# Kernel optimization log

Hardware: AMD Instinct MI355X
Metric: run time of the kernel (lower is better)

The kernel has to match this reference:

```python
import jax, jax.numpy as jnp
import numpy as np

B, H, S, D = 2, 16, 2048, 128
BLOCK_N = 64          # key-block size used by the Triton inner loop (BLOCK_N<=HEAD_DIM configs)
CAUSAL = True
NEG = -1000000.0      # kernel masks with -1e6, not -inf
LOG2E = 1.44269504


def _round_away(x):
    # tl.math.floor(|x| + 0.5) * sign(x): round half away from zero
    return jnp.floor(jnp.abs(x) + 0.5) * jnp.where(x >= 0, 1.0, -1.0)


def _quant_per_token(x):
    # per-(B,H,S) symmetric int8 quantization (values kept in fp32; exact, since |q|<=127)
    amax = jnp.maximum(jnp.max(jnp.abs(x), axis=-1), 1e-8)
    scale = amax / 127.0
    xq = jnp.clip(_round_away(x / scale[..., None]), -127.0, 127.0)
    return xq, scale


def _quant_per_head(v):
    # per-(B,H) symmetric int8 quantization
    amax = jnp.maximum(jnp.max(jnp.abs(v), axis=(-2, -1)), 1e-8)
    scale = amax / 127.0
    vq = jnp.clip(_round_away(v / scale[..., None, None]), -127.0, 127.0)
    return vq, scale


def _forward(q, k, v, sm_scale):
    q_q, q_s = _quant_per_token(q)   # [B,H,S,D], [B,H,S]
    k_q, k_s = _quant_per_token(k)
    v_q, v_s = _quant_per_head(v)    # [B,H,S,D], [B,H]

    nb = S // BLOCK_N
    k_blk = k_q.reshape(B, H, nb, BLOCK_N, D).transpose(2, 0, 1, 3, 4)   # [nb,B,H,Bn,D]
    ks_blk = k_s.reshape(B, H, nb, BLOCK_N).transpose(2, 0, 1, 3)        # [nb,B,H,Bn]
    v_blk = v_q.reshape(B, H, nb, BLOCK_N, D).transpose(2, 0, 1, 3, 4)   # [nb,B,H,Bn,D]
    cols = jnp.arange(S, dtype=jnp.int32).reshape(nb, BLOCK_N)
    rows = jnp.arange(S, dtype=jnp.int32)

    qk_scale = sm_scale * LOG2E
    vs_term = v_s[:, :, None, None] / 127.0  # [B,H,1,1]

    def step(carry, xs):
        m, l, acc = carry
        kb, ksb, vb, cb = xs
        # int8 QK^T dequantized: exact in fp32 (|sum| <= 127*127*128 < 2^24)
        qk = jnp.einsum('bhsd,bhnd->bhsn', q_q, kb)
        qk = qk * q_s[..., None] * ksb[:, :, None, :] * qk_scale
        if CAUSAL:
            qk = jnp.where(rows[:, None] >= cb[None, :], qk, NEG)
        m_new = jnp.maximum(m, jnp.max(qk, axis=-1))
        p = jnp.exp2(qk - m_new[..., None])
        # online quantization of probabilities at block-local running max (as in kernel)
        p_q = jnp.floor(p * 127.0 + 0.5)
        alpha = jnp.exp2(m - m_new)
        l = l * alpha + jnp.sum(p, axis=-1)
        acc = acc * alpha[..., None] + jnp.einsum('bhsn,bhnd->bhsd', p_q, vb) * vs_term
        return (m_new, l, acc), None

    m0 = jnp.full((B, H, S), -jnp.inf, dtype=jnp.float32)
    l0 = jnp.ones((B, H, S), dtype=jnp.float32)   # killed by alpha=exp2(-inf)=0 at first block
    acc0 = jnp.zeros((B, H, S, D), dtype=jnp.float32)
    (m, l, acc), _ = jax.lax.scan(jax.checkpoint(step), (m0, l0, acc0),
                                  (k_blk, ks_blk, v_blk, cols))
    return acc / l[..., None]


def setup_inputs() -> dict:
    key = jax.random.key(0)
    kq, kk, kv = jax.random.split(key, 3)
    q = jax.random.normal(kq, (B, H, S, D), dtype=jnp.float32)
    k = jax.random.normal(kk, (B, H, S, D), dtype=jnp.float32)
    v = jax.random.normal(kv, (B, H, S, D), dtype=jnp.float32)
    sm_scale = jnp.float32(1.0 / np.sqrt(D))
    return {"q": q, "k": k, "v": v, "sm_scale": sm_scale}


def reference(q, k, v, sm_scale):
    return _forward(q, k, v, sm_scale)
```

## Files before the change

kernel.cpp:

```cpp
#include <hip/hip_runtime.h>

#define S_LEN 2048
#define D_DIM 128
#define NBH   32
#define LOG2E 1.44269504f
#define NEGM  -1000000.0f

typedef __bf16 bf16x8 __attribute__((ext_vector_type(8)));
typedef short  s16x8  __attribute__((ext_vector_type(8)));
typedef float  f32x4  __attribute__((ext_vector_type(4)));
typedef float  f32x16 __attribute__((ext_vector_type(16)));
typedef unsigned int u32x4 __attribute__((ext_vector_type(4)));

static __device__ __forceinline__ unsigned short f32_to_bf16_bits_exact(float f) {
    return (unsigned short)(__float_as_uint(f) >> 16);
}
static __device__ __forceinline__ float round_away(float t) {
    float r = floorf(fabsf(t) + 0.5f);
    return (t >= 0.0f) ? r : -r;
}
static __device__ __forceinline__ unsigned int pq_pack(float p0, float p1) {
    float a = floorf(fmaf(p0, 127.0f, 0.5f));
    float b = floorf(fmaf(p1, 127.0f, 0.5f));
    return __builtin_amdgcn_perm(__float_as_uint(b), __float_as_uint(a), 0x07060302);
}

__global__ __launch_bounds__(256) void quant_qkv_kernel(
    const float* __restrict__ q, const float* __restrict__ k,
    const float* __restrict__ v,
    unsigned short* __restrict__ qq, unsigned short* __restrict__ kq,
    float* __restrict__ qs, float* __restrict__ ks,
    unsigned int* __restrict__ vab)
{
    if (blockIdx.x < 16384) {
        const int R = NBH * S_LEN;
        int w   = blockIdx.x * 8 + (threadIdx.x >> 5);
        int l32 = threadIdx.x & 31;
        const float* src; unsigned short* dq; float* ds; int row;
        if (w < R) { src = q; dq = qq; ds = qs; row = w; }
        else       { src = k; dq = kq; ds = ks; row = w - R; }
        size_t base = (size_t)row * D_DIM + l32 * 4;
        float4 x = *(const float4*)(src + base);
        float amax = fmaxf(fmaxf(fabsf(x.x), fabsf(x.y)), fmaxf(fabsf(x.z), fabsf(x.w)));
        #pragma unroll
        for (int m = 1; m < 32; m <<= 1) amax = fmaxf(amax, __shfl_xor(amax, m));
        float scale = fmaxf(amax, 1e-8f) / 127.0f;
        ushort4 o;
        o.x = f32_to_bf16_bits_exact(fminf(fmaxf(round_away(x.x / scale), -127.0f), 127.0f));
        o.y = f32_to_bf16_bits_exact(fminf(fmaxf(round_away(x.y / scale), -127.0f), 127.0f));
        o.z = f32_to_bf16_bits_exact(fminf(fmaxf(round_away(x.z / scale), -127.0f), 127.0f));
        o.w = f32_to_bf16_bits_exact(fminf(fmaxf(round_away(x.w / scale), -127.0f), 127.0f));
        *(ushort4*)(dq + base) = o;
        if (l32 == 0) ds[row] = scale;
    } else {
        int bid2 = blockIdx.x - 16384;
        int bh = bid2 >> 3, blk = bid2 & 7;
        const float4* base = (const float4*)(v + (size_t)bh * S_LEN * D_DIM) + blk * 8192;
        int t = threadIdx.x;
        float am = 0.0f;
        #pragma unroll
        for (int i = 0; i < 32; ++i) {
            float4 x = base[t + i * 256];
            am = fmaxf(am, fmaxf(fmaxf(fabsf(x.x), fabsf(x.y)), fmaxf(fabsf(x.z), fabsf(x.w))));
        }
        #pragma unroll
        for (int m = 1; m < 64; m <<= 1) am = fmaxf(am, __shfl_xor(am, m));
        __shared__ float red[4];
        if ((t & 63) == 0) red[t >> 6] = am;
        __syncthreads();
        if (t == 0) {
            float a = fmaxf(fmaxf(red[0], red[1]), fmaxf(red[2], red[3]));
            atomicMax(&vab[bh], __float_as_uint(a));
        }
    }
}

__global__ __launch_bounds__(256) void vtq_kernel(const float* __restrict__ v,
                                                  const unsigned int* __restrict__ vab,
                                                  unsigned short* __restrict__ vT)
{
    __shared__ unsigned short tileT[128][72];
    int bh = blockIdx.x >> 5, sb = blockIdx.x & 31;
    float scale = fmaxf(__uint_as_float(vab[bh]), 1e-8f) / 127.0f;
    int t = threadIdx.x;
    const float* src = v + ((size_t)bh * S_LEN + sb * 64) * D_DIM;
    #pragma unroll
    for (int it = 0; it < 8; ++it) {
        int c = t + it * 256;
        int rs = c >> 5, c4 = (c & 31) * 4;
        float4 x = *(const float4*)(src + rs * D_DIM + c4);
        float vals[4] = {x.x, x.y, x.z, x.w};
        #pragma unroll
        for (int u = 0; u < 4; ++u) {
            float r = fminf(fmaxf(round_away(vals[u] / scale), -127.0f), 127.0f);
            tileT[c4 + u][rs] = f32_to_bf16_bits_exact(r);
        }
    }
    __syncthreads();
    unsigned short* dst = vT + (size_t)bh * D_DIM * S_LEN + sb * 64;
    #pragma unroll
    for (int it = 0; it < 4; ++it) {
        int c = t + it * 256;
        int d = c >> 3, c8 = (c & 7) * 8;
        *(s16x8*)(dst + (size_t)d * S_LEN + c8) = *(const s16x8*)&tileT[d][c8];
    }
}

__global__ __launch_bounds__(512, 4) void attn_kernel(
    const unsigned short* __restrict__ qq,
    const unsigned short* __restrict__ kq,
    const unsigned short* __restrict__ vT,
    const float* __restrict__ qs,
    const float* __restrict__ ks,
    const unsigned int* __restrict__ vab,
    const float* __restrict__ smp,
    float* __restrict__ out)
{
    extern __shared__ char smem[];

    const int tid  = threadIdx.x;
    const int lane = tid & 63;
    const int wid  = tid >> 6;
    const int w4   = wid & 3;
    const int half = wid >> 2;
    const int c32  = lane & 31;
    const int hi   = lane >> 5;
    const int t8   = tid & 255;

    char*   KbH  = smem + half * 8192;
    char*   VbH  = smem + 16384 + half * 8192;
    float*  ksl  = (float*)(smem + 32768);
    float2* ML   = (float2*)(smem + 34816);
    char*   Qlds = smem + 40960;
    float*  Ol   = (float*)smem;

    const int bid = blockIdx.x;
    const int g   = bid >> 5;
    const int qb  = (g < 8) ? (15 - g) : (g - 8);
    const int bh  = bid & 31;

    const float qk_scale = smp[0] * LOG2E;
    const float vscale   = fmaxf(__uint_as_float(vab[bh]), 1e-8f) / 127.0f;
    const float vs_term  = vscale / 127.0f;

    const int   q  = qb * 128 + c32 * 4 + w4;
    const float qf = qs[(size_t)bh * S_LEN + q] * qk_scale;

    const char* kqb = (const char*)(kq + (size_t)bh * S_LEN * D_DIM);
    const char* vtb = (const char*)(vT + (size_t)bh * D_DIM * S_LEN);

    ((f32x4*)ksl)[tid] = ((const f32x4*)(ks + (size_t)bh * S_LEN))[tid];
    {
        const char* qqb = (const char*)(qq + ((size_t)bh * S_LEN + qb * 128) * D_DIM);
        #pragma unroll
        for (int it = 0; it < 4; ++it) {
            int L = (tid + it * 512) * 16;
            int w = L >> 13, Lw = L & 8191;
            int r = Lw >> 8, x = Lw & 255;
            int col = x ^ ((r & 15) << 4);
            *(s16x8*)(Qlds + L) = *(const s16x8*)(qqb + (r * 4 + w) * 256 + col);
        }
    }

    int kOff[2], vOff[2], lOff[2];
    #pragma unroll
    for (int it = 0; it < 2; ++it) {
        int L = (t8 + it * 256) * 16;
        lOff[it] = L;
        int r = L >> 8, x = L & 255;
        int c = x ^ ((r & 15) << 4);
        kOff[it] = (half * 32 + r) * 256 + c;
        vOff[it] = ((c >> 6) * 32 + r) * (S_LEN * 2) + half * 64 + (c & 63);
    }

    float mrow = -100.0f;
    float lrow = 0.0f;
    f32x16 oacc0, oacc1, oacc2, oacc3;
    #pragma unroll
    for (int i = 0; i < 16; ++i) { oacc0[i] = 0.f; oacc1[i] = 0.f; oacc2[i] = 0.f; oacc3[i] = 0.f; }

    const int swz = (c32 & 15) << 4;
    const char* aBase = KbH + c32 * 256;
    const char* bBase = Qlds + w4 * 8192 + c32 * 256;
    const char* vBase = VbH + c32 * 256;

    const int jn = 2 * qb + 2;
    for (int j = 0; j < jn; ++j) {
        const int jb = j * 64;
        s16x8 kr0 = *(const s16x8*)(kqb + jb * 256 + kOff[0]);
        s16x8 kr1 = *(const s16x8*)(kqb + jb * 256 + kOff[1]);
        s16x8 vr0 = *(const s16x8*)(vtb + jb * 2   + vOff[0]);
        s16x8 vr1 = *(const s16x8*)(vtb + jb * 2   + vOff[1]);
        __syncthreads();
        *(s16x8*)(KbH + lOff[0]) = kr0;
        *(s16x8*)(KbH + lOff[1]) = kr1;
        *(s16x8*)(VbH + lOff[0]) = vr0;
        *(s16x8*)(VbH + lOff[1]) = vr1;
        __syncthreads();

        f32x16 sc;
        #pragma unroll
        for (int i = 0; i < 16; ++i) sc[i] = 0.f;
        #pragma unroll
        for (int st = 0; st < 8; ++st) {
            int cB = (st * 32 + hi * 16) ^ swz;
            bf16x8 a = __builtin_bit_cast(bf16x8, *(const s16x8*)(aBase + cB));
            bf16x8 b = __builtin_bit_cast(bf16x8, *(const s16x8*)(bBase + cB));
            sc = __builtin_amdgcn_mfma_f32_32x32x16_bf16(a, b, sc, 0, 0, 0);
        }

        const int  jbh = jb + half * 32;
        const bool need_mask = (jbh + 31 > qb * 128 + w4);
        float mhA = -3.0e38f, mhB = -3.0e38f;
        #pragma unroll
        for (int gg = 0; gg < 4; ++gg) {
            f32x4 kv = *(const f32x4*)&ksl[jbh + gg * 8 + hi * 4];
            #pragma unroll
            for (int i = 0; i < 4; ++i) {
                int r = gg * 4 + i;
                float c  = qf * kv[i];
                float tv = fmaf(sc[r], c, -mrow);
                if (need_mask) tv = (q >= jbh + gg * 8 + i + hi * 4) ? tv : NEGM;
                sc[r] = tv;
                if (i & 1) mhB = fmaxf(mhB, tv);
                else       mhA = fmaxf(mhA, tv);
            }
        }
        float mh     = fmaxf(mhA, mhB);
        float vmax_t = fmaxf(mh, __shfl_xor(mh, 32));

        if (__any(vmax_t > 1.0f)) {
            float sh    = fmaxf(vmax_t, 0.0f);
            float alpha = exp2f(-sh);
            mrow += sh;
            #pragma unroll
            for (int r = 0; r < 16; ++r) sc[r] -= sh;
            oacc0 *= alpha; oacc1 *= alpha; oacc2 *= alpha; oacc3 *= alpha;
            lrow  *= alpha;
        }

        float ts[8];
        #pragma unroll
        for (int r = 0; r < 8; ++r) {
            sc[r]     = exp2f(sc[r]);
            sc[r + 8] = exp2f(sc[r + 8]);
            ts[r] = sc[r] + sc[r + 8];
        }
        #pragma unroll
        for (int stp = 4; stp >= 1; stp >>= 1)
            #pragma unroll
            for (int r = 0; r < stp; ++r) ts[r] += ts[r + stp];
        lrow += ts[0] + __shfl_xor(ts[0], 32);

        unsigned int W[8];
        #pragma unroll
        for (int gg = 0; gg < 4; ++gg) {
            W[gg*2+0] = pq_pack(sc[gg*4+0], sc[gg*4+1]);
            W[gg*2+1] = pq_pack(sc[gg*4+2], sc[gg*4+3]);
        }
        #pragma unroll
        for (int s = 0; s < 2; ++s) {
            asm("v_permlane32_swap_b32 %0, %1" : "+v"(W[s*4+0]), "+v"(W[s*4+2]));
            asm("v_permlane32_swap_b32 %0, %1" : "+v"(W[s*4+1]), "+v"(W[s*4+3]));
        }
        #pragma unroll
        for (int s = 0; s < 2; ++s) {
            u32x4 uw; uw.x = W[s*4+0]; uw.y = W[s*4+1]; uw.z = W[s*4+2]; uw.w = W[s*4+3];
            bf16x8 bfrag = __builtin_bit_cast(bf16x8, uw);
            int cb = s * 32 + hi * 16;
            bf16x8 va;
            va = __builtin_bit_cast(bf16x8, *(const s16x8*)(vBase + ((cb +   0) ^ swz)));
            oacc0 = __builtin_amdgcn_mfma_f32_32x32x16_bf16(va, bfrag, oacc0, 0, 0, 0);
            va = __builtin_bit_cast(bf16x8, *(const s16x8*)(vBase + ((cb +  64) ^ swz)));
            oacc1 = __builtin_amdgcn_mfma_f32_32x32x16_bf16(va, bfrag, oacc1, 0, 0, 0);
            va = __builtin_bit_cast(bf16x8, *(const s16x8*)(vBase + ((cb + 128) ^ swz)));
            oacc2 = __builtin_amdgcn_mfma_f32_32x32x16_bf16(va, bfrag, oacc2, 0, 0, 0);
            va = __builtin_bit_cast(bf16x8, *(const s16x8*)(vBase + ((cb + 192) ^ swz)));
            oacc3 = __builtin_amdgcn_mfma_f32_32x32x16_bf16(va, bfrag, oacc3, 0, 0, 0);
        }
    }

    __syncthreads();
    if (hi == 0) { float2 ml2; ml2.x = mrow; ml2.y = lrow; ML[half * 128 + w4 * 32 + c32] = ml2; }
    __syncthreads();
    float2 mo  = ML[(1 - half) * 128 + w4 * 32 + c32];
    float  mfin = fmaxf(mrow, mo.x);
    float  bs  = exp2f(mrow - mfin);
    float  bo  = exp2f(mo.x - mfin);
    float  lfin = lrow * bs + mo.y * bo;
    const float inv = bs * vs_term / lfin;

    for (int pass = 0; pass < 2; ++pass) {
        __syncthreads();
        if (half == 0 && (w4 >> 1) == pass) {
            float* reg = Ol + (w4 & 1) * 4224 + c32 * 132;
            #pragma unroll
            for (int r = 0; r < 16; ++r) {
                int drow = (r & 3) + 8 * (r >> 2) + 4 * hi;
                reg[drow]      = oacc0[r] * inv;
                reg[drow + 32] = oacc1[r] * inv;
                reg[drow + 64] = oacc2[r] * inv;
                reg[drow + 96] = oacc3[r] * inv;
            }
        }
        __syncthreads();
        if (half == 1 && (w4 >> 1) == pass) {
            float* reg = Ol + (w4 & 1) * 4224 + c32 * 132;
            #pragma unroll
            for (int r = 0; r < 16; ++r) {
                int drow = (r & 3) + 8 * (r >> 2) + 4 * hi;
                reg[drow]      += oacc0[r] * inv;
                reg[drow + 32] += oacc1[r] * inv;
                reg[drow + 64] += oacc2[r] * inv;
                reg[drow + 96] += oacc3[r] * inv;
            }
        }
        __syncthreads();
        #pragma unroll
        for (int it = 0; it < 4; ++it) {
            int idx = tid + it * 512;
            int w2  = idx >> 10;
            int rem = idx & 1023;
            int row = rem >> 5, c4 = rem & 31;
            f32x4 v4 = *(const f32x4*)(Ol + w2 * 4224 + row * 132 + c4 * 4);
            int qr = qb * 128 + row * 4 + pass * 2 + w2;
            *(f32x4*)(out + ((size_t)bh * S_LEN + qr) * D_DIM + c4 * 4) = v4;
        }
    }
}

extern "C" void kernel_launch(void* const* d_in, const int* in_sizes, int n_in,
                              void* d_out, int out_size, void* d_ws, size_t ws_size,
                              hipStream_t stream)
{
    const float* q  = (const float*)d_in[0];
    const float* k  = (const float*)d_in[1];
    const float* v  = (const float*)d_in[2];
    const float* sm = (const float*)d_in[3];

    if (ws_size < (size_t)50857000) return;
    char* ws = (char*)d_ws;
    unsigned short* qq = (unsigned short*)(ws);
    unsigned short* kq = (unsigned short*)(ws + (1u << 24));
    unsigned short* vT = (unsigned short*)(ws + (2u << 24));
    float*          qs = (float*)(ws + (3u << 24));
    float*          ks = (float*)(ws + (3u << 24) + 262144);
    unsigned int*  vab = (unsigned int*)(ws + (3u << 24) + 524288);
    float*         out = (float*)d_out;

    hipFuncSetAttribute((const void*)attn_kernel,
                        hipFuncAttributeMaxDynamicSharedMemorySize, 73728);

    hipMemsetAsync(vab, 0, NBH * sizeof(unsigned int), stream);
    quant_qkv_kernel<<<dim3(16640), dim3(256), 0, stream>>>(q, k, v, qq, kq, qs, ks, vab);
    vtq_kernel<<<dim3(1024), dim3(256), 0, stream>>>(v, vab, vT);
    attn_kernel<<<dim3(512), dim3(512), 73728, stream>>>(qq, kq, vT, qs, ks, vab, sm, out);
}
```

Before: 125.8 us.

## Fuse Q quantization into attention and split long causal rows across blocks

Q quantization moves from the separate prepass into the attention kernel, which now reads fp32 Q, quantizes it into LDS and stores the per-row scales there. This removes the qq/qs round trip through global memory. Query blocks 9-15, the longest causal rows, are each split into two key-range chunks processed by separate workgroups (736 blocks instead of 512) to even out work. The chunk that finishes last, found through an atomic ticket, merges both partial outputs using the stored m/l values. In exchange this adds scratch traffic, atomics and merge work, and each workgroup repeats the Q quantization.

```diff
diff --git a/kernel.cpp b/kernel.cpp
--- a/kernel.cpp
+++ b/kernel.cpp
@@ -11,6 +11,7 @@
 typedef float  f32x4  __attribute__((ext_vector_type(4)));
 typedef float  f32x16 __attribute__((ext_vector_type(16)));
 typedef unsigned int u32x4 __attribute__((ext_vector_type(4)));
+typedef unsigned int u32x2 __attribute__((ext_vector_type(2)));
 
 static __device__ __forceinline__ unsigned short f32_to_bf16_bits_exact(float f) {
     return (unsigned short)(__float_as_uint(f) >> 16);
@@ -25,22 +26,16 @@
     return __builtin_amdgcn_perm(__float_as_uint(b), __float_as_uint(a), 0x07060302);
 }
 
-__global__ __launch_bounds__(256) void quant_qkv_kernel(
-    const float* __restrict__ q, const float* __restrict__ k,
-    const float* __restrict__ v,
-    unsigned short* __restrict__ qq, unsigned short* __restrict__ kq,
-    float* __restrict__ qs, float* __restrict__ ks,
+__global__ __launch_bounds__(256) void quant_kv_kernel(
+    const float* __restrict__ k, const float* __restrict__ v,
+    unsigned short* __restrict__ kq, float* __restrict__ ks,
     unsigned int* __restrict__ vab)
 {
-    if (blockIdx.x < 16384) {
-        const int R = NBH * S_LEN;
-        int w   = blockIdx.x * 8 + (threadIdx.x >> 5);
+    if (blockIdx.x < 8192) {
+        int row = blockIdx.x * 8 + (threadIdx.x >> 5);
         int l32 = threadIdx.x & 31;
-        const float* src; unsigned short* dq; float* ds; int row;
-        if (w < R) { src = q; dq = qq; ds = qs; row = w; }
-        else       { src = k; dq = kq; ds = ks; row = w - R; }
         size_t base = (size_t)row * D_DIM + l32 * 4;
-        float4 x = *(const float4*)(src + base);
+        float4 x = *(const float4*)(k + base);
         float amax = fmaxf(fmaxf(fabsf(x.x), fabsf(x.y)), fmaxf(fabsf(x.z), fabsf(x.w)));
         #pragma unroll
         for (int m = 1; m < 32; m <<= 1) amax = fmaxf(amax, __shfl_xor(amax, m));
@@ -50,10 +45,10 @@
         o.y = f32_to_bf16_bits_exact(fminf(fmaxf(round_away(x.y / scale), -127.0f), 127.0f));
         o.z = f32_to_bf16_bits_exact(fminf(fmaxf(round_away(x.z / scale), -127.0f), 127.0f));
         o.w = f32_to_bf16_bits_exact(fminf(fmaxf(round_away(x.w / scale), -127.0f), 127.0f));
-        *(ushort4*)(dq + base) = o;
-        if (l32 == 0) ds[row] = scale;
+        *(ushort4*)(kq + base) = o;
+        if (l32 == 0) ks[row] = scale;
     } else {
-        int bid2 = blockIdx.x - 16384;
+        int bid2 = blockIdx.x - 8192;
         int bh = bid2 >> 3, blk = bid2 & 7;
         const float4* base = (const float4*)(v + (size_t)bh * S_LEN * D_DIM) + blk * 8192;
         int t = threadIdx.x;
@@ -107,14 +102,16 @@
 }
 
 __global__ __launch_bounds__(512, 4) void attn_kernel(
-    const unsigned short* __restrict__ qq,
+    const float* __restrict__ qsrc,
     const unsigned short* __restrict__ kq,
     const unsigned short* __restrict__ vT,
-    const float* __restrict__ qs,
     const float* __restrict__ ks,
     const unsigned int* __restrict__ vab,
     const float* __restrict__ smp,
-    float* __restrict__ out)
+    float* __restrict__ out,
+    float* __restrict__ U1,
+    float2* __restrict__ mlbuf,
+    unsigned int* __restrict__ tickets)
 {
     extern __shared__ char smem[];
 
@@ -134,33 +131,63 @@
     char*   Qlds = smem + 40960;
     float*  Ol   = (float*)smem;
 
-    const int bid = blockIdx.x;
-    const int g   = bid >> 5;
-    const int qb  = (g < 8) ? (15 - g) : (g - 8);
-    const int bh  = bid & 31;
+    int rem = (int)blockIdx.x, qb = 0, chunk = -1, bh = 0;
+    {
+        bool fnd = false;
+        for (int L = 18; L >= 2 && !fnd; --L) {
+            if (L >= 10 && L <= 16) {
+                if (rem < 64) { qb = L - 1; chunk = rem >> 5; bh = rem & 31; fnd = true; }
+                else rem -= 64;
+            }
+            if (!fnd && !(L & 1)) {
+                int qu = (L >> 1) - 1;
+                if (qu <= 8) {
+                    if (rem < 32) { qb = qu; chunk = -1; bh = rem & 31; fnd = true; }
+                    else rem -= 32;
+                }
+            }
+        }
+    }
+    int j0 = 0, jEnd = 2 * qb + 2;
+    if (chunk == 0) jEnd = qb + 1;
+    else if (chunk == 1) j0 = qb + 1;
+    const int pair = (qb - 9) * 32 + bh;
 
     const float qk_scale = smp[0] * LOG2E;
     const float vscale   = fmaxf(__uint_as_float(vab[bh]), 1e-8f) / 127.0f;
     const float vs_term  = vscale / 127.0f;
 
-    const int   q  = qb * 128 + c32 * 4 + w4;
-    const float qf = qs[(size_t)bh * S_LEN + q] * qk_scale;
-
     const char* kqb = (const char*)(kq + (size_t)bh * S_LEN * D_DIM);
     const char* vtb = (const char*)(vT + (size_t)bh * D_DIM * S_LEN);
 
     ((f32x4*)ksl)[tid] = ((const f32x4*)(ks + (size_t)bh * S_LEN))[tid];
+    float* qsl = (float*)smem;
     {
-        const char* qqb = (const char*)(qq + ((size_t)bh * S_LEN + qb * 128) * D_DIM);
-        #pragma unroll
-        for (int it = 0; it < 4; ++it) {
-            int L = (tid + it * 512) * 16;
-            int w = L >> 13, Lw = L & 8191;
-            int r = Lw >> 8, x = Lw & 255;
-            int col = x ^ ((r & 15) << 4);
-            *(s16x8*)(Qlds + L) = *(const s16x8*)(qqb + (r * 4 + w) * 256 + col);
-        }
-    }
+        const float* qg = qsrc + ((size_t)bh * S_LEN + qb * 128) * D_DIM;
+        int l32 = tid & 31;
+        #pragma unroll
+        for (int p = 0; p < 8; ++p) {
+            int row = p * 16 + (tid >> 5);
+            f32x4 x = *(const f32x4*)(qg + (size_t)row * D_DIM + l32 * 4);
+            float am = fmaxf(fmaxf(fabsf(x[0]), fabsf(x[1])), fmaxf(fabsf(x[2]), fabsf(x[3])));
+            #pragma unroll
+            for (int m = 1; m < 32; m <<= 1) am = fmaxf(am, __shfl_xor(am, m));
+            float scale = fmaxf(am, 1e-8f) / 127.0f;
+            if (l32 == 0) qsl[row] = scale;
+            unsigned short b0 = f32_to_bf16_bits_exact(fminf(fmaxf(round_away(x[0] / scale), -127.0f), 127.0f));
+            unsigned short b1 = f32_to_bf16_bits_exact(fminf(fmaxf(round_away(x[1] / scale), -127.0f), 127.0f));
+            unsigned short b2 = f32_to_bf16_bits_exact(fminf(fmaxf(round_away(x[2] / scale), -127.0f), 127.0f));
+            unsigned short b3 = f32_to_bf16_bits_exact(fminf(fmaxf(round_away(x[3] / scale), -127.0f), 127.0f));
+            u32x2 pk; pk.x = (unsigned int)b0 | ((unsigned int)b1 << 16);
+            pk.y = (unsigned int)b2 | ((unsigned int)b3 << 16);
+            int base = (row & 3) * 8192 + (row >> 2) * 256;
+            int off  = (l32 * 8) ^ (((row >> 2) & 15) << 4);
+            *(u32x2*)(Qlds + base + off) = pk;
+        }
+    }
+    __syncthreads();
+    const int   q  = qb * 128 + c32 * 4 + w4;
+    const float qf = qsl[c32 * 4 + w4] * qk_scale;
 
     int kOff[2], vOff[2], lOff[2];
     #pragma unroll
@@ -184,8 +211,7 @@
     const char* bBase = Qlds + w4 * 8192 + c32 * 256;
     const char* vBase = VbH + c32 * 256;
 
-    const int jn = 2 * qb + 2;
-    for (int j = 0; j < jn; ++j) {
+    for (int j = j0; j < jEnd; ++j) {
         const int jb = j * 64;
         s16x8 kr0 = *(const s16x8*)(kqb + jb * 256 + kOff[0]);
         s16x8 kr1 = *(const s16x8*)(kqb + jb * 256 + kOff[1]);
@@ -288,7 +314,15 @@
     float  bs  = exp2f(mrow - mfin);
     float  bo  = exp2f(mo.x - mfin);
     float  lfin = lrow * bs + mo.y * bo;
-    const float inv = bs * vs_term / lfin;
+
+    if (chunk >= 0 && half == 0 && hi == 0) {
+        float2 t; t.x = mfin; t.y = lfin;
+        mlbuf[(size_t)pair * 256 + chunk * 128 + (c32 * 4 + w4)] = t;
+    }
+
+    const float inv = (chunk < 0) ? (bs * vs_term / lfin) : bs;
+    float* dstBase = (chunk == 1) ? (U1 + (size_t)pair * 16384)
+                                  : (out + ((size_t)bh * S_LEN + qb * 128) * D_DIM);
 
     for (int pass = 0; pass < 2; ++pass) {
         __syncthreads();
@@ -320,11 +354,44 @@
         for (int it = 0; it < 4; ++it) {
             int idx = tid + it * 512;
             int w2  = idx >> 10;
-            int rem = idx & 1023;
-            int row = rem >> 5, c4 = rem & 31;
+            int rem2 = idx & 1023;
+            int row = rem2 >> 5, c4 = rem2 & 31;
             f32x4 v4 = *(const f32x4*)(Ol + w2 * 4224 + row * 132 + c4 * 4);
-            int qr = qb * 128 + row * 4 + pass * 2 + w2;
-            *(f32x4*)(out + ((size_t)bh * S_LEN + qr) * D_DIM + c4 * 4) = v4;
+            int lr = row * 4 + pass * 2 + w2;
+            *(f32x4*)(dstBase + (size_t)lr * D_DIM + c4 * 4) = v4;
+        }
+    }
+
+    if (chunk >= 0) {
+        __syncthreads();
+        int* flg = (int*)(smem + 34816);
+        if (tid == 0) {
+            __threadfence();
+            unsigned int old = __hip_atomic_fetch_add(&tickets[pair], 1u,
+                                 __ATOMIC_ACQ_REL, __HIP_MEMORY_SCOPE_AGENT);
+            flg[0] = (int)old;
+        }
+        __syncthreads();
+        if (flg[0] == 1) {
+            __threadfence();
+            const float2* mp = mlbuf + (size_t)pair * 256;
+            float* orows = out + ((size_t)bh * S_LEN + qb * 128) * D_DIM;
+            const float* U1p = U1 + (size_t)pair * 16384;
+            #pragma unroll
+            for (int it = 0; it < 8; ++it) {
+                int vec = tid + it * 512;
+                int row = vec >> 5;
+                float2 a = mp[row], b = mp[128 + row];
+                float ms = fmaxf(a.x, b.x);
+                float w0 = exp2f(a.x - ms), w1 = exp2f(b.x - ms);
+                float scl = vs_term / (w0 * a.y + w1 * b.y);
+                f32x4 u0 = ((const f32x4*)orows)[vec];
+                f32x4 u1 = ((const f32x4*)U1p)[vec];
+                f32x4 r;
+                #pragma unroll
+                for (int c = 0; c < 4; ++c) r[c] = (u0[c] * w0 + u1[c] * w1) * scl;
+                ((f32x4*)orows)[vec] = r;
+            }
         }
     }
 }
@@ -340,19 +407,21 @@
 
     if (ws_size < (size_t)50857000) return;
     char* ws = (char*)d_ws;
-    unsigned short* qq = (unsigned short*)(ws);
-    unsigned short* kq = (unsigned short*)(ws + (1u << 24));
-    unsigned short* vT = (unsigned short*)(ws + (2u << 24));
-    float*          qs = (float*)(ws + (3u << 24));
-    float*          ks = (float*)(ws + (3u << 24) + 262144);
-    unsigned int*  vab = (unsigned int*)(ws + (3u << 24) + 524288);
+    unsigned short* kq = (unsigned short*)(ws);
+    unsigned short* vT = (unsigned short*)(ws + (1u << 24));
+    float*          ks = (float*)(ws + (2u << 24));
+    unsigned int*  vab = (unsigned int*)(ws + (2u << 24) + 262144);
+    unsigned int* tick = (unsigned int*)(ws + (2u << 24) + 263168);
+    float2*         ml = (float2*)(ws + (2u << 24) + 264192);
+    float*          U1 = (float*)(ws + (2u << 24) + 1048576);
     float*         out = (float*)d_out;
 
     hipFuncSetAttribute((const void*)attn_kernel,
                         hipFuncAttributeMaxDynamicSharedMemorySize, 73728);
 
-    hipMemsetAsync(vab, 0, NBH * sizeof(unsigned int), stream);
-    quant_qkv_kernel<<<dim3(16640), dim3(256), 0, stream>>>(q, k, v, qq, kq, qs, ks, vab);
+    hipMemsetAsync(ws + (2u << 24) + 262144, 0, 2048, stream);
+    quant_kv_kernel<<<dim3(8448), dim3(256), 0, stream>>>(k, v, kq, ks, vab);
     vtq_kernel<<<dim3(1024), dim3(256), 0, stream>>>(v, vab, vT);
-    attn_kernel<<<dim3(512), dim3(512), 73728, stream>>>(qq, kq, vT, qs, ks, vab, sm, out);
-}
+    attn_kernel<<<dim3(736), dim3(512), 73728, stream>>>(q, kq, vT, ks, vab, sm,
+                                                         out, U1, ml, tick);
+}
```

New measurement: 219.0 us. 74.1% more time.

## Double key block size to 128 and prefetch next K/V block into registers

Applied to the files above, without the earlier changes.

Each iteration of the attention kernel now processes a 128-key block, 64 keys per half, with two score accumulators per wave. This halves the number of barrier-synchronised iterations. Global loads for the next K/V block are issued into registers before the compute of the current block, to overlap memory latency with MFMA work. Only the last block takes the masked path, and the block ordering becomes a simple descending schedule. The cost is more LDS (about 106 KB) and more registers, with launch bounds reduced to 2 blocks per SM, which lowers occupancy.

```diff
diff --git a/kernel.cpp b/kernel.cpp
--- a/kernel.cpp
+++ b/kernel.cpp
@@ -106,7 +106,7 @@
     }
 }
 
-__global__ __launch_bounds__(512, 4) void attn_kernel(
+__global__ __launch_bounds__(512, 2) void attn_kernel(
     const unsigned short* __restrict__ qq,
     const unsigned short* __restrict__ kq,
     const unsigned short* __restrict__ vT,
@@ -127,16 +127,15 @@
     const int hi   = lane >> 5;
     const int t8   = tid & 255;
 
-    char*   KbH  = smem + half * 8192;
-    char*   VbH  = smem + 16384 + half * 8192;
-    float*  ksl  = (float*)(smem + 32768);
-    float2* ML   = (float2*)(smem + 34816);
-    char*   Qlds = smem + 40960;
+    char*   KbH  = smem + half * 16384;
+    char*   VbH  = smem + 32768 + half * 16384;
+    float*  ksl  = (float*)(smem + 65536);
+    float2* ML   = (float2*)(smem + 73728);
+    char*   Qlds = smem + 75776;
     float*  Ol   = (float*)smem;
 
     const int bid = blockIdx.x;
-    const int g   = bid >> 5;
-    const int qb  = (g < 8) ? (15 - g) : (g - 8);
+    const int qb  = 15 - (bid >> 5);
     const int bh  = bid & 31;
 
     const float qk_scale = smp[0] * LOG2E;
@@ -162,15 +161,17 @@
         }
     }
 
-    int kOff[2], vOff[2], lOff[2];
-    #pragma unroll
-    for (int it = 0; it < 2; ++it) {
+    int kOff[4], vOff[4], lOff[4];
+    #pragma unroll
+    for (int it = 0; it < 4; ++it) {
         int L = (t8 + it * 256) * 16;
         lOff[it] = L;
         int r = L >> 8, x = L & 255;
         int c = x ^ ((r & 15) << 4);
-        kOff[it] = (half * 32 + r) * 256 + c;
-        vOff[it] = ((c >> 6) * 32 + r) * (S_LEN * 2) + half * 64 + (c & 63);
+        kOff[it] = (half * 64 + r) * 256 + c;
+        int rho = L >> 9, xv = L & 511;
+        int cv  = xv ^ ((rho & 15) << 4);
+        vOff[it] = ((cv >> 7) * 32 + rho) * (S_LEN * 2) + half * 128 + (cv & 127);
     }
 
     float mrow = -100.0f;
@@ -182,48 +183,65 @@
     const int swz = (c32 & 15) << 4;
     const char* aBase = KbH + c32 * 256;
     const char* bBase = Qlds + w4 * 8192 + c32 * 256;
-    const char* vBase = VbH + c32 * 256;
-
-    const int jn = 2 * qb + 2;
-    for (int j = 0; j < jn; ++j) {
-        const int jb = j * 64;
-        s16x8 kr0 = *(const s16x8*)(kqb + jb * 256 + kOff[0]);
-        s16x8 kr1 = *(const s16x8*)(kqb + jb * 256 + kOff[1]);
-        s16x8 vr0 = *(const s16x8*)(vtb + jb * 2   + vOff[0]);
-        s16x8 vr1 = *(const s16x8*)(vtb + jb * 2   + vOff[1]);
-        __syncthreads();
-        *(s16x8*)(KbH + lOff[0]) = kr0;
-        *(s16x8*)(KbH + lOff[1]) = kr1;
-        *(s16x8*)(VbH + lOff[0]) = vr0;
-        *(s16x8*)(VbH + lOff[1]) = vr1;
-        __syncthreads();
-
-        f32x16 sc;
-        #pragma unroll
-        for (int i = 0; i < 16; ++i) sc[i] = 0.f;
+    const char* vBase = VbH + c32 * 512;
+
+    const int jn_d = qb + 1;
+
+    s16x8 kpre[4], vpre[4];
+    #pragma unroll
+    for (int it = 0; it < 4; ++it) {
+        kpre[it] = *(const s16x8*)(kqb + kOff[it]);
+        vpre[it] = *(const s16x8*)(vtb + vOff[it]);
+    }
+
+    auto iter = [&](const int d, const bool domask) __attribute__((always_inline)) {
+        __syncthreads();
+        #pragma unroll
+        for (int it = 0; it < 4; ++it) *(s16x8*)(KbH + lOff[it]) = kpre[it];
+        #pragma unroll
+        for (int it = 0; it < 4; ++it) *(s16x8*)(VbH + lOff[it]) = vpre[it];
+        if (d + 1 < jn_d) {
+            const int jb2 = (d + 1) * 128;
+            #pragma unroll
+            for (int it = 0; it < 4; ++it) {
+                kpre[it] = *(const s16x8*)(kqb + jb2 * 256 + kOff[it]);
+                vpre[it] = *(const s16x8*)(vtb + jb2 * 2   + vOff[it]);
+            }
+        }
+        __syncthreads();
+
+        f32x16 sc0, sc1;
+        #pragma unroll
+        for (int i = 0; i < 16; ++i) { sc0[i] = 0.f; sc1[i] = 0.f; }
         #pragma unroll
         for (int st = 0; st < 8; ++st) {
             int cB = (st * 32 + hi * 16) ^ swz;
-            bf16x8 a = __builtin_bit_cast(bf16x8, *(const s16x8*)(aBase + cB));
-            bf16x8 b = __builtin_bit_cast(bf16x8, *(const s16x8*)(bBase + cB));
-            sc = __builtin_amdgcn_mfma_f32_32x32x16_bf16(a, b, sc, 0, 0, 0);
-        }
-
-        const int  jbh = jb + half * 32;
-        const bool need_mask = (jbh + 31 > qb * 128 + w4);
+            bf16x8 a0 = __builtin_bit_cast(bf16x8, *(const s16x8*)(aBase + cB));
+            bf16x8 a1 = __builtin_bit_cast(bf16x8, *(const s16x8*)(aBase + 32 * 256 + cB));
+            bf16x8 b  = __builtin_bit_cast(bf16x8, *(const s16x8*)(bBase + cB));
+            sc0 = __builtin_amdgcn_mfma_f32_32x32x16_bf16(a0, b, sc0, 0, 0, 0);
+            sc1 = __builtin_amdgcn_mfma_f32_32x32x16_bf16(a1, b, sc1, 0, 0, 0);
+        }
+
+        const int jbh = d * 128 + half * 64;
         float mhA = -3.0e38f, mhB = -3.0e38f;
         #pragma unroll
         for (int gg = 0; gg < 4; ++gg) {
-            f32x4 kv = *(const f32x4*)&ksl[jbh + gg * 8 + hi * 4];
+            f32x4 kv0 = *(const f32x4*)&ksl[jbh + gg * 8 + hi * 4];
+            f32x4 kv1 = *(const f32x4*)&ksl[jbh + 32 + gg * 8 + hi * 4];
             #pragma unroll
             for (int i = 0; i < 4; ++i) {
                 int r = gg * 4 + i;
-                float c  = qf * kv[i];
-                float tv = fmaf(sc[r], c, -mrow);
-                if (need_mask) tv = (q >= jbh + gg * 8 + i + hi * 4) ? tv : NEGM;
-                sc[r] = tv;
-                if (i & 1) mhB = fmaxf(mhB, tv);
-                else       mhA = fmaxf(mhA, tv);
+                float tv0 = fmaf(sc0[r], qf * kv0[i], -mrow);
+                float tv1 = fmaf(sc1[r], qf * kv1[i], -mrow);
+                if (domask) {
+                    int key0 = jbh + gg * 8 + i + hi * 4;
+                    tv0 = (q >= key0)      ? tv0 : NEGM;
+                    tv1 = (q >= key0 + 32) ? tv1 : NEGM;
+                }
+                sc0[r] = tv0; sc1[r] = tv1;
+                if (i & 1) mhB = fmaxf(mhB, fmaxf(tv0, tv1));
+                else       mhA = fmaxf(mhA, fmaxf(tv0, tv1));
             }
         }
         float mh     = fmaxf(mhA, mhB);
@@ -234,7 +252,7 @@
             float alpha = exp2f(-sh);
             mrow += sh;
             #pragma unroll
-            for (int r = 0; r < 16; ++r) sc[r] -= sh;
+            for (int r = 0; r < 16; ++r) { sc0[r] -= sh; sc1[r] -= sh; }
             oacc0 *= alpha; oacc1 *= alpha; oacc2 *= alpha; oacc3 *= alpha;
             lrow  *= alpha;
         }
@@ -242,9 +260,11 @@
         float ts[8];
         #pragma unroll
         for (int r = 0; r < 8; ++r) {
-            sc[r]     = exp2f(sc[r]);
-            sc[r + 8] = exp2f(sc[r + 8]);
-            ts[r] = sc[r] + sc[r + 8];
+            sc0[r]     = exp2f(sc0[r]);
+            sc0[r + 8] = exp2f(sc0[r + 8]);
+            sc1[r]     = exp2f(sc1[r]);
+            sc1[r + 8] = exp2f(sc1[r + 8]);
+            ts[r] = (sc0[r] + sc0[r + 8]) + (sc1[r] + sc1[r + 8]);
         }
         #pragma unroll
         for (int stp = 4; stp >= 1; stp >>= 1)
@@ -252,33 +272,44 @@
             for (int r = 0; r < stp; ++r) ts[r] += ts[r + stp];
         lrow += ts[0] + __shfl_xor(ts[0], 32);
 
-        unsigned int W[8];
+        unsigned int W0[8], W1[8];
         #pragma unroll
         for (int gg = 0; gg < 4; ++gg) {
-            W[gg*2+0] = pq_pack(sc[gg*4+0], sc[gg*4+1]);
-            W[gg*2+1] = pq_pack(sc[gg*4+2], sc[gg*4+3]);
+            W0[gg*2+0] = pq_pack(sc0[gg*4+0], sc0[gg*4+1]);
+            W0[gg*2+1] = pq_pack(sc0[gg*4+2], sc0[gg*4+3]);
+            W1[gg*2+0] = pq_pack(sc1[gg*4+0], sc1[gg*4+1]);
+            W1[gg*2+1] = pq_pack(sc1[gg*4+2], sc1[gg*4+3]);
         }
         #pragma unroll
         for (int s = 0; s < 2; ++s) {
-            asm("v_permlane32_swap_b32 %0, %1" : "+v"(W[s*4+0]), "+v"(W[s*4+2]));
-            asm("v_permlane32_swap_b32 %0, %1" : "+v"(W[s*4+1]), "+v"(W[s*4+3]));
-        }
-        #pragma unroll
-        for (int s = 0; s < 2; ++s) {
-            u32x4 uw; uw.x = W[s*4+0]; uw.y = W[s*4+1]; uw.z = W[s*4+2]; uw.w = W[s*4+3];
-            bf16x8 bfrag = __builtin_bit_cast(bf16x8, uw);
-            int cb = s * 32 + hi * 16;
-            bf16x8 va;
-            va = __builtin_bit_cast(bf16x8, *(const s16x8*)(vBase + ((cb +   0) ^ swz)));
-            oacc0 = __builtin_amdgcn_mfma_f32_32x32x16_bf16(va, bfrag, oacc0, 0, 0, 0);
-            va = __builtin_bit_cast(bf16x8, *(const s16x8*)(vBase + ((cb +  64) ^ swz)));
-            oacc1 = __builtin_amdgcn_mfma_f32_32x32x16_bf16(va, bfrag, oacc1, 0, 0, 0);
-            va = __builtin_bit_cast(bf16x8, *(const s16x8*)(vBase + ((cb + 128) ^ swz)));
-            oacc2 = __builtin_amdgcn_mfma_f32_32x32x16_bf16(va, bfrag, oacc2, 0, 0, 0);
-            va = __builtin_bit_cast(bf16x8, *(const s16x8*)(vBase + ((cb + 192) ^ swz)));
-            oacc3 = __builtin_amdgcn_mfma_f32_32x32x16_bf16(va, bfrag, oacc3, 0, 0, 0);
-        }
-    }
+            asm("v_permlane32_swap_b32 %0, %1" : "+v"(W0[s*4+0]), "+v"(W0[s*4+2]));
+            asm("v_permlane32_swap_b32 %0, %1" : "+v"(W0[s*4+1]), "+v"(W0[s*4+3]));
+            asm("v_permlane32_swap_b32 %0, %1" : "+v"(W1[s*4+0]), "+v"(W1[s*4+2]));
+            asm("v_permlane32_swap_b32 %0, %1" : "+v"(W1[s*4+1]), "+v"(W1[s*4+3]));
+        }
+        #pragma unroll
+        for (int t = 0; t < 2; ++t) {
+            const unsigned int* Wt = t ? W1 : W0;
+            #pragma unroll
+            for (int s = 0; s < 2; ++s) {
+                u32x4 uw; uw.x = Wt[s*4+0]; uw.y = Wt[s*4+1]; uw.z = Wt[s*4+2]; uw.w = Wt[s*4+3];
+                bf16x8 bfrag = __builtin_bit_cast(bf16x8, uw);
+                int cb = t * 64 + s * 32 + hi * 16;
+                bf16x8 va;
+                va = __builtin_bit_cast(bf16x8, *(const s16x8*)(vBase + ((cb +   0) ^ swz)));
+                oacc0 = __builtin_amdgcn_mfma_f32_32x32x16_bf16(va, bfrag, oacc0, 0, 0, 0);
+                va = __builtin_bit_cast(bf16x8, *(const s16x8*)(vBase + ((cb + 128) ^ swz)));
+                oacc1 = __builtin_amdgcn_mfma_f32_32x32x16_bf16(va, bfrag, oacc1, 0, 0, 0);
+                va = __builtin_bit_cast(bf16x8, *(const s16x8*)(vBase + ((cb + 256) ^ swz)));
+                oacc2 = __builtin_amdgcn_mfma_f32_32x32x16_bf16(va, bfrag, oacc2, 0, 0, 0);
+                va = __builtin_bit_cast(bf16x8, *(const s16x8*)(vBase + ((cb + 384) ^ swz)));
+                oacc3 = __builtin_amdgcn_mfma_f32_32x32x16_bf16(va, bfrag, oacc3, 0, 0, 0);
+            }
+        }
+    };
+
+    for (int d = 0; d < jn_d - 1; ++d) iter(d, false);
+    iter(jn_d - 1, true);
 
     __syncthreads();
     if (hi == 0) { float2 ml2; ml2.x = mrow; ml2.y = lrow; ML[half * 128 + w4 * 32 + c32] = ml2; }
@@ -349,10 +380,10 @@
     float*         out = (float*)d_out;
 
     hipFuncSetAttribute((const void*)attn_kernel,
-                        hipFuncAttributeMaxDynamicSharedMemorySize, 73728);
+                        hipFuncAttributeMaxDynamicSharedMemorySize, 108544);
 
     hipMemsetAsync(vab, 0, NBH * sizeof(unsigned int), stream);
     quant_qkv_kernel<<<dim3(16640), dim3(256), 0, stream>>>(q, k, v, qq, kq, qs, ks, vab);
     vtq_kernel<<<dim3(1024), dim3(256), 0, stream>>>(v, vab, vT);
-    attn_kernel<<<dim3(512), dim3(512), 73728, stream>>>(qq, kq, vT, qs, ks, vab, sm, out);
-}
+    attn_kernel<<<dim3(512), dim3(512), 108544, stream>>>(qq, kq, vT, qs, ks, vab, sm, out);
+}
```

New measurement: 111.1 us, median of 2. 11.7% less time.
